# Kernel optimization log

Hardware: AMD Instinct MI355X
Metric: run time of the kernel (lower is better)

Reference implementation:

```python
import jax, jax.numpy as jnp
import numpy as np

B, C, Q, D = 64, 512, 64, 256  # D = 2 * hidden_size; similarity weight has 3*D = 768 entries


def _length_mask(key, batch, seqlen):
    # realistic padding masks: each row has a random valid prefix length in [seqlen//2, seqlen]
    lens = jax.random.randint(key, (batch,), seqlen // 2, seqlen + 1)
    return (jnp.arange(seqlen)[None, :] < lens[:, None]).astype(jnp.int32)


def setup_inputs() -> dict:
    key = jax.random.key(0)
    k1, k2, k3, k4, k5 = jax.random.split(key, 5)
    context = jax.random.normal(k1, (B, C, D), dtype=jnp.float32)
    question = jax.random.normal(k2, (B, Q, D), dtype=jnp.float32)
    context_mask = _length_mask(k3, B, C)
    question_mask = _length_mask(k4, B, Q)
    w = jax.random.normal(k5, (3 * D,), dtype=jnp.float32) * (1.0 / np.sqrt(3 * D))
    return {"context": context, "question": question,
            "context_mask": context_mask, "question_mask": question_mask, "w": w}


def reference(context, question, context_mask, question_mask, w):
    d = context.shape[-1]
    # Linear([c, q, c*q]) with no bias decomposes exactly into three terms.
    w_c, w_q, w_m = w[:d], w[d:2 * d], w[2 * d:]
    sim = ((context @ w_c)[:, :, None]                      # [B, C, 1]
           + (question @ w_q)[:, None, :]                   # [B, 1, Q]
           + jnp.einsum('bcd,bqd->bcq', context * w_m, question))  # [B, C, Q]
    neg = jnp.finfo(sim.dtype).min
    # context-to-query attention (mask question positions)
    sim_q = jnp.where(question_mask[:, None, :] != 0, sim, neg)
    a = jax.nn.softmax(sim_q, axis=2)                        # [B, C, Q]
    c2q = jnp.einsum('bcq,bqd->bcd', a, question)            # [B, C, D]
    # query-to-context attention (max over Q, mask context positions)
    sim_max = jnp.max(sim, axis=2)                           # [B, C]
    sim_max = jnp.where(context_mask != 0, sim_max, neg)
    b = jax.nn.softmax(sim_max, axis=1)                      # [B, C]
    q2c = jnp.einsum('bc,bcd->bd', b, context)[:, None, :]   # [B, 1, D]
    q2c = jnp.broadcast_to(q2c, context.shape)               # [B, C, D]
    g = jnp.concatenate([context, c2q, context * c2q, context * q2c], axis=-1)
    return g
```

## Files before the change

kernel.cpp:

```cpp
#include <hip/hip_runtime.h>
#include <hip/hip_bf16.h>
#include <float.h>

#define B_ 64
#define C_ 512
#define Q_ 64
#define D_ 256

typedef _Float16 f16x8 __attribute__((ext_vector_type(8)));
typedef float f32x4 __attribute__((ext_vector_type(4)));

union U4H8 { uint4 u; f16x8 h; };
union UH2 { _Float16 h[2]; uint32_t u; };

__device__ __forceinline__ uint32_t packh2(float a, float b) {
  UH2 v; v.h[0] = (_Float16)a; v.h[1] = (_Float16)b; return v.u;
}

__device__ __forceinline__ float wred_sum(float v) {
#pragma unroll
  for (int off = 32; off > 0; off >>= 1) v += __shfl_xor(v, off, 64);
  return v;
}
__device__ __forceinline__ float wred_max(float v) {
#pragma unroll
  for (int off = 32; off > 0; off >>= 1) v = fmaxf(v, __shfl_xor(v, off, 64));
  return v;
}

__global__ __launch_bounds__(256) void k_rowdot(const float* __restrict__ src,
                                                const float* __restrict__ wgt,
                                                float* __restrict__ out, int nrows) {
  int wv = threadIdx.x >> 6, ln = threadIdx.x & 63;
  int row = blockIdx.x * 4 + wv;
  if (row >= nrows) return;
  float4 s4 = *(const float4*)(src + (size_t)row * D_ + 4 * ln);
  float4 w4 = *(const float4*)(wgt + 4 * ln);
  float p = s4.x * w4.x + s4.y * w4.y + s4.z * w4.z + s4.w * w4.w;
  p = wred_sum(p);
  if (ln == 0) out[row] = p;
}

__global__ __launch_bounds__(256, 3) void k_main(
    const float* __restrict__ ctx, const float* __restrict__ qst,
    const int* __restrict__ qmask, const float* __restrict__ w,
    const float* __restrict__ qwq_g, float* __restrict__ g,
    float* __restrict__ simmax_g) {
  __shared__ __align__(16) ushort qbuf[Q_ * D_];
  __shared__ __align__(16) ushort pbuf[4][16 * Q_];
  __shared__ float qwq_l[Q_];
  __shared__ int   qml_l[Q_];

  const int bid = blockIdx.x;
  const int b = bid & 63;
  const int c0 = (bid >> 6) * 64;
  const int t = threadIdx.x;
  const int wv = t >> 6, ln = t & 63;
  const int lc = ln & 15;
  const int lg = ln >> 4;
  const int c0w = c0 + wv * 16;

  f16x8 bfrag[8];
  float cwc_p = 0.f;
  const float* crow = ctx + ((size_t)b * C_ + c0w + lc) * D_;
  float* grow0 = g + ((size_t)b * C_ + c0w + lc) * (4 * D_);
#pragma unroll
  for (int kk = 0; kk < 8; ++kk) {
    int kb = kk * 32 + lg * 8;
    float4 cv0 = *(const float4*)(crow + kb);
    float4 cv1 = *(const float4*)(crow + kb + 4);
    float4 wc0 = *(const float4*)(w + kb);
    float4 wc1 = *(const float4*)(w + kb + 4);
    float4 wm0 = *(const float4*)(w + 2 * D_ + kb);
    float4 wm1 = *(const float4*)(w + 2 * D_ + kb + 4);
    cwc_p += cv0.x * wc0.x + cv0.y * wc0.y + cv0.z * wc0.z + cv0.w * wc0.w
           + cv1.x * wc1.x + cv1.y * wc1.y + cv1.z * wc1.z + cv1.w * wc1.w;
    bfrag[kk][0] = (_Float16)(cv0.x * wm0.x);
    bfrag[kk][1] = (_Float16)(cv0.y * wm0.y);
    bfrag[kk][2] = (_Float16)(cv0.z * wm0.z);
    bfrag[kk][3] = (_Float16)(cv0.w * wm0.w);
    bfrag[kk][4] = (_Float16)(cv1.x * wm1.x);
    bfrag[kk][5] = (_Float16)(cv1.y * wm1.y);
    bfrag[kk][6] = (_Float16)(cv1.z * wm1.z);
    bfrag[kk][7] = (_Float16)(cv1.w * wm1.w);
    *(float4*)(grow0 + kb) = cv0;
    *(float4*)(grow0 + kb + 4) = cv1;
  }
  float cwc = cwc_p;
  cwc += __shfl_xor(cwc, 16, 64);
  cwc += __shfl_xor(cwc, 32, 64);

  const float* qb = qst + (size_t)b * Q_ * D_;
#pragma unroll 4
  for (int it = 0; it < 32; ++it) {
    int idx = it * 256 + t;
    int q = idx >> 7, jp = idx & 127;
    float2 v = *(const float2*)(qb + q * D_ + 2 * jp);
    int ch = jp >> 2;
    int phys = (ch & ~7) | ((ch & 7) ^ (q & 7));
    *(uint32_t*)((char*)qbuf + q * 512 + phys * 16 + (jp & 3) * 4) = packh2(v.x, v.y);
  }
  if (t < Q_) { qwq_l[t] = qwq_g[b * Q_ + t]; qml_l[t] = qmask[b * Q_ + t]; }
  __syncthreads();

  f32x4 sacc[4];
#pragma unroll
  for (int tq = 0; tq < 4; ++tq) sacc[tq] = f32x4{0.f, 0.f, 0.f, 0.f};
#pragma unroll
  for (int tq = 0; tq < 4; ++tq) {
    int q = 16 * tq + lc;
#pragma unroll
    for (int kk = 0; kk < 8; ++kk) {
      int ch = lg + 4 * kk;
      int phys = (ch & ~7) | ((ch & 7) ^ (q & 7));
      U4H8 a; a.u = *(const uint4*)((const char*)qbuf + q * 512 + phys * 16);
      sacc[tq] = __builtin_amdgcn_mfma_f32_16x16x32_f16(a.h, bfrag[kk], sacc[tq], 0, 0, 0);
    }
  }

  float vals[4][4];
  float rmax = -FLT_MAX;
#pragma unroll
  for (int tq = 0; tq < 4; ++tq) {
    float4 qw4 = *(const float4*)(qwq_l + 16 * tq + 4 * lg);
#pragma unroll
    for (int r = 0; r < 4; ++r) {
      float qv = (r == 0) ? qw4.x : (r == 1) ? qw4.y : (r == 2) ? qw4.z : qw4.w;
      vals[tq][r] = sacc[tq][r] + cwc + qv;
      rmax = fmaxf(rmax, vals[tq][r]);
    }
  }
  rmax = fmaxf(rmax, __shfl_xor(rmax, 16, 64));
  rmax = fmaxf(rmax, __shfl_xor(rmax, 32, 64));
  if (ln < 16) simmax_g[b * C_ + c0w + lc] = rmax;

  float mmax = -FLT_MAX;
#pragma unroll
  for (int tq = 0; tq < 4; ++tq) {
    int4 qm4 = *(const int4*)(qml_l + 16 * tq + 4 * lg);
#pragma unroll
    for (int r = 0; r < 4; ++r) {
      int m = (r == 0) ? qm4.x : (r == 1) ? qm4.y : (r == 2) ? qm4.z : qm4.w;
      vals[tq][r] = m ? vals[tq][r] : -FLT_MAX;
      mmax = fmaxf(mmax, vals[tq][r]);
    }
  }
  mmax = fmaxf(mmax, __shfl_xor(mmax, 16, 64));
  mmax = fmaxf(mmax, __shfl_xor(mmax, 32, 64));
  float esum = 0.f;
#pragma unroll
  for (int tq = 0; tq < 4; ++tq)
#pragma unroll
    for (int r = 0; r < 4; ++r) {
      vals[tq][r] = __expf(vals[tq][r] - mmax);
      esum += vals[tq][r];
    }
  esum += __shfl_xor(esum, 16, 64);
  esum += __shfl_xor(esum, 32, 64);
  float inv = 1.f / esum;
#pragma unroll
  for (int tq = 0; tq < 4; ++tq) {
    uint32_t p01 = packh2(vals[tq][0] * inv, vals[tq][1] * inv);
    uint32_t p23 = packh2(vals[tq][2] * inv, vals[tq][3] * inv);
    int qb4 = 16 * tq + 4 * lg;
    int phys = ((qb4 >> 3) ^ (lc & 7));
    char* dst = (char*)pbuf[wv] + lc * 128 + phys * 16 + (qb4 & 7) * 2;
    *(uint2*)dst = uint2{p01, p23};
  }
  __syncthreads();

#pragma unroll 4
  for (int it = 0; it < 32; ++it) {
    int q = t & 63;
    int jp = (t >> 6) + 4 * it;
    float2 v = *(const float2*)(qb + q * D_ + 2 * jp);
    int d0 = 2 * jp, d1 = d0 + 1;
    UH2 h0; h0.h[0] = (_Float16)v.x;
    UH2 h1; h1.h[0] = (_Float16)v.y;
    *(ushort*)((char*)qbuf + d0 * 128 + (((q >> 3) ^ (d0 & 7)) << 4) + (q & 7) * 2) = (ushort)(h0.u & 0xffff);
    *(ushort*)((char*)qbuf + d1 * 128 + (((q >> 3) ^ (d1 & 7)) << 4) + (q & 7) * 2) = (ushort)(h1.u & 0xffff);
  }
  __syncthreads();

  f16x8 pfragB[2];
#pragma unroll
  for (int ks = 0; ks < 2; ++ks) {
    int phys = (lg + 4 * ks) ^ (lc & 7);
    U4H8 a; a.u = *(const uint4*)((const char*)pbuf[wv] + lc * 128 + phys * 16);
    pfragB[ks] = a.h;
  }
  const float* crow2 = ctx + ((size_t)b * C_ + c0w + lc) * D_;
  float* grow = g + ((size_t)b * C_ + c0w + lc) * (4 * D_);
#pragma unroll 4
  for (int dt = 0; dt < 16; ++dt) {
    f32x4 acc = f32x4{0.f, 0.f, 0.f, 0.f};
#pragma unroll
    for (int ks = 0; ks < 2; ++ks) {
      int d = dt * 16 + lc;
      int phys = (lg + 4 * ks) ^ (d & 7);
      U4H8 aq; aq.u = *(const uint4*)((const char*)qbuf + d * 128 + phys * 16);
      acc = __builtin_amdgcn_mfma_f32_16x16x32_f16(aq.h, pfragB[ks], acc, 0, 0, 0);
    }
    int dcol = dt * 16 + 4 * lg;
    float4 cvv = *(const float4*)(crow2 + dcol);
    float4 c2qv{acc[0], acc[1], acc[2], acc[3]};
    *(float4*)(grow + D_ + dcol) = c2qv;
    float4 p2{cvv.x * c2qv.x, cvv.y * c2qv.y, cvv.z * c2qv.z, cvv.w * c2qv.w};
    *(float4*)(grow + 2 * D_ + dcol) = p2;
  }
}

__global__ __launch_bounds__(256) void k_q2c_bs(const float* __restrict__ ctx,
                                                const float* __restrict__ simmax,
                                                const int* __restrict__ cmask,
                                                float* __restrict__ part) {
  int b = blockIdx.x, ch = blockIdx.y, t = threadIdx.x;
  int wv = t >> 6, ln = t & 63;
  __shared__ float bls[C_];
  __shared__ float sred[4];
  __shared__ float ssum[4];
  float v0 = simmax[b * C_ + t], v1 = simmax[b * C_ + 256 + t];
  if (!cmask[b * C_ + t]) v0 = -FLT_MAX;
  if (!cmask[b * C_ + 256 + t]) v1 = -FLT_MAX;
  float mx = wred_max(fmaxf(v0, v1));
  if (ln == 0) sred[wv] = mx;
  __syncthreads();
  float bm = fmaxf(fmaxf(sred[0], sred[1]), fmaxf(sred[2], sred[3]));
  float e0 = __expf(v0 - bm), e1 = __expf(v1 - bm);
  float ps = wred_sum(e0 + e1);
  if (ln == 0) ssum[wv] = ps;
  __syncthreads();
  float bs = ssum[0] + ssum[1] + ssum[2] + ssum[3];
  float invbs = 1.f / bs;
  bls[t] = e0 * invbs;
  bls[256 + t] = e1 * invbs;
  __syncthreads();
  float acc = 0.f;
  int cbeg = ch * 64;
#pragma unroll 4
  for (int c = cbeg; c < cbeg + 64; ++c)
    acc += bls[c] * ctx[((size_t)b * C_ + c) * D_ + t];
  part[((size_t)b * 8 + ch) * D_ + t] = acc;
}

__global__ __launch_bounds__(256) void k_q2c_sum(const float* __restrict__ part,
                                                 float* __restrict__ q2c) {
  int b = blockIdx.x, t = threadIdx.x;
  float s = 0.f;
#pragma unroll
  for (int ch = 0; ch < 8; ++ch) s += part[((size_t)b * 8 + ch) * D_ + t];
  q2c[b * D_ + t] = s;
}

__global__ __launch_bounds__(256) void k_g3(const float* __restrict__ ctx,
                                            const float* __restrict__ q2c,
                                            float* __restrict__ g) {
  size_t i = (size_t)blockIdx.x * 256 + threadIdx.x;
  int d4 = (int)(i & 63);
  size_t row = i >> 6;
  int b = (int)(row >> 9);
  float4 cv = *(const float4*)(ctx + row * D_ + 4 * d4);
  float4 qv = *(const float4*)(q2c + (size_t)b * D_ + 4 * d4);
  float4 o{cv.x * qv.x, cv.y * qv.y, cv.z * qv.z, cv.w * qv.w};
  *(float4*)(g + row * (4 * D_) + 3 * D_ + 4 * d4) = o;
}

extern "C" void kernel_launch(void* const* d_in, const int* in_sizes, int n_in,
                              void* d_out, int out_size, void* d_ws, size_t ws_size,
                              hipStream_t stream) {
  const float* ctx   = (const float*)d_in[0];
  const float* qst   = (const float*)d_in[1];
  const int*   cmask = (const int*)d_in[2];
  const int*   qmask = (const int*)d_in[3];
  const float* w     = (const float*)d_in[4];
  float* g  = (float*)d_out;
  float* ws = (float*)d_ws;

  float* qwq    = ws;
  float* simmax = ws + 4096;
  float* part   = ws + 36864;
  float* q2c    = ws + 167936;

  k_rowdot<<<dim3(B_ * Q_ / 4), 256, 0, stream>>>(qst, w + D_, qwq, B_ * Q_);
  k_main<<<dim3(512), 256, 0, stream>>>(ctx, qst, qmask, w, qwq, g, simmax);
  k_q2c_bs<<<dim3(B_, 8), 256, 0, stream>>>(ctx, simmax, cmask, part);
  k_q2c_sum<<<dim3(B_), 256, 0, stream>>>(part, q2c);
  k_g3<<<dim3(B_ * C_ * 64 / 256), 256, 0, stream>>>(ctx, q2c, g);
}
```

Measured before the change: 68.42 us.

## Fuse question-weight dot into main kernel and merge q2c sum with g3 write

Computes the question·w_q row dots inside k_main from the fp16 question tile already staged in shared memory, removing the separate k_rowdot launch. It also folds the q2c partial reduction into the final g[...,3D:] writer, so five launches become three. The cost is that the dot now uses fp16-rounded question values, which adds some error, and each of the eight chunk blocks per batch redoes the partial sum. The launch bound on k_main also drops its min-blocks hint of 3.

Result: slower. 70.55 us (+3.1%).

```diff
diff --git a/kernel.cpp b/kernel.cpp
--- a/kernel.cpp
+++ b/kernel.cpp
@@ -16,6 +16,10 @@
 __device__ __forceinline__ uint32_t packh2(float a, float b) {
   UH2 v; v.h[0] = (_Float16)a; v.h[1] = (_Float16)b; return v.u;
 }
+__device__ __forceinline__ float2 h2f2(uint32_t u) {
+  UH2 v; v.u = u;
+  float2 r; r.x = (float)v.h[0]; r.y = (float)v.h[1]; return r;
+}
 
 __device__ __forceinline__ float wred_sum(float v) {
 #pragma unroll
@@ -28,24 +32,10 @@
   return v;
 }
 
-__global__ __launch_bounds__(256) void k_rowdot(const float* __restrict__ src,
-                                                const float* __restrict__ wgt,
-                                                float* __restrict__ out, int nrows) {
-  int wv = threadIdx.x >> 6, ln = threadIdx.x & 63;
-  int row = blockIdx.x * 4 + wv;
-  if (row >= nrows) return;
-  float4 s4 = *(const float4*)(src + (size_t)row * D_ + 4 * ln);
-  float4 w4 = *(const float4*)(wgt + 4 * ln);
-  float p = s4.x * w4.x + s4.y * w4.y + s4.z * w4.z + s4.w * w4.w;
-  p = wred_sum(p);
-  if (ln == 0) out[row] = p;
-}
-
-__global__ __launch_bounds__(256, 3) void k_main(
+__global__ __launch_bounds__(256) void k_main(
     const float* __restrict__ ctx, const float* __restrict__ qst,
     const int* __restrict__ qmask, const float* __restrict__ w,
-    const float* __restrict__ qwq_g, float* __restrict__ g,
-    float* __restrict__ simmax_g) {
+    float* __restrict__ g, float* __restrict__ simmax_g) {
   __shared__ __align__(16) ushort qbuf[Q_ * D_];
   __shared__ __align__(16) ushort pbuf[4][16 * Q_];
   __shared__ float qwq_l[Q_];
@@ -100,7 +90,28 @@
     int phys = (ch & ~7) | ((ch & 7) ^ (q & 7));
     *(uint32_t*)((char*)qbuf + q * 512 + phys * 16 + (jp & 3) * 4) = packh2(v.x, v.y);
   }
-  if (t < Q_) { qwq_l[t] = qwq_g[b * Q_ + t]; qml_l[t] = qmask[b * Q_ + t]; }
+  if (t < Q_) qml_l[t] = qmask[b * Q_ + t];
+  __syncthreads();
+
+  {
+    const int q = t >> 2, s4 = t & 3;
+    float qp = 0.f;
+#pragma unroll
+    for (int jj = 0; jj < 8; ++jj) {
+      int ch = s4 * 8 + jj;
+      int phys = (ch & ~7) | ((ch & 7) ^ (q & 7));
+      U4H8 a; a.u = *(const uint4*)((const char*)qbuf + q * 512 + phys * 16);
+      int d0 = ch * 8;
+      float4 w0 = *(const float4*)(w + D_ + d0);
+      float4 w1 = *(const float4*)(w + D_ + d0 + 4);
+      float2 f0 = h2f2(a.u.x), f1 = h2f2(a.u.y), f2 = h2f2(a.u.z), f3 = h2f2(a.u.w);
+      qp += f0.x * w0.x + f0.y * w0.y + f1.x * w0.z + f1.y * w0.w
+          + f2.x * w1.x + f2.y * w1.y + f3.x * w1.z + f3.y * w1.w;
+    }
+    qp += __shfl_xor(qp, 1, 64);
+    qp += __shfl_xor(qp, 2, 64);
+    if ((t & 3) == 0) qwq_l[q] = qp;
+  }
   __syncthreads();
 
   f32x4 sacc[4];
@@ -243,26 +254,26 @@
   part[((size_t)b * 8 + ch) * D_ + t] = acc;
 }
 
-__global__ __launch_bounds__(256) void k_q2c_sum(const float* __restrict__ part,
-                                                 float* __restrict__ q2c) {
-  int b = blockIdx.x, t = threadIdx.x;
+__global__ __launch_bounds__(256) void k_g3q(const float* __restrict__ ctx,
+                                             const float* __restrict__ part,
+                                             float* __restrict__ g) {
+  int b = blockIdx.x, ch = blockIdx.y, t = threadIdx.x;
+  __shared__ float q2c_l[D_];
   float s = 0.f;
 #pragma unroll
-  for (int ch = 0; ch < 8; ++ch) s += part[((size_t)b * 8 + ch) * D_ + t];
-  q2c[b * D_ + t] = s;
-}
-
-__global__ __launch_bounds__(256) void k_g3(const float* __restrict__ ctx,
-                                            const float* __restrict__ q2c,
-                                            float* __restrict__ g) {
-  size_t i = (size_t)blockIdx.x * 256 + threadIdx.x;
-  int d4 = (int)(i & 63);
-  size_t row = i >> 6;
-  int b = (int)(row >> 9);
-  float4 cv = *(const float4*)(ctx + row * D_ + 4 * d4);
-  float4 qv = *(const float4*)(q2c + (size_t)b * D_ + 4 * d4);
-  float4 o{cv.x * qv.x, cv.y * qv.y, cv.z * qv.z, cv.w * qv.w};
-  *(float4*)(g + row * (4 * D_) + 3 * D_ + 4 * d4) = o;
+  for (int k = 0; k < 8; ++k) s += part[((size_t)b * 8 + k) * D_ + t];
+  q2c_l[t] = s;
+  __syncthreads();
+  int d4 = t & 63;
+  int ro = t >> 6;
+  float4 qv = *(const float4*)(q2c_l + 4 * d4);
+#pragma unroll 4
+  for (int it = 0; it < 16; ++it) {
+    int c = ch * 64 + it * 4 + ro;
+    float4 cv = *(const float4*)(ctx + ((size_t)b * C_ + c) * D_ + 4 * d4);
+    float4 o{cv.x * qv.x, cv.y * qv.y, cv.z * qv.z, cv.w * qv.w};
+    *(float4*)(g + ((size_t)b * C_ + c) * (4 * D_) + 3 * D_ + 4 * d4) = o;
+  }
 }
 
 extern "C" void kernel_launch(void* const* d_in, const int* in_sizes, int n_in,
@@ -276,14 +287,10 @@
   float* g  = (float*)d_out;
   float* ws = (float*)d_ws;
 
-  float* qwq    = ws;
-  float* simmax = ws + 4096;
-  float* part   = ws + 36864;
-  float* q2c    = ws + 167936;
-
-  k_rowdot<<<dim3(B_ * Q_ / 4), 256, 0, stream>>>(qst, w + D_, qwq, B_ * Q_);
-  k_main<<<dim3(512), 256, 0, stream>>>(ctx, qst, qmask, w, qwq, g, simmax);
+  float* simmax = ws;
+  float* part   = ws + 32768;
+
+  k_main<<<dim3(512), 256, 0, stream>>>(ctx, qst, qmask, w, g, simmax);
   k_q2c_bs<<<dim3(B_, 8), 256, 0, stream>>>(ctx, simmax, cmask, part);
-  k_q2c_sum<<<dim3(B_), 256, 0, stream>>>(part, q2c);
-  k_g3<<<dim3(B_ * C_ * 64 / 256), 256, 0, stream>>>(ctx, q2c, g);
-}
+  k_g3q<<<dim3(B_, 8), 256, 0, stream>>>(ctx, part, g);
+}
```
